# Performance work log

Measured on AMD Instinct MI355X. Metric: run time of the kernel, lower is better.

The kernel has to match this reference:

```python
import jax, jax.numpy as jnp
import numpy as np

INPUT_DIM = 512


def setup_inputs() -> dict:
    key = jax.random.key(0)
    ks = jax.random.split(key, 9)
    B = 262144
    d = INPUT_DIM
    inp = {
        "combined": jax.random.normal(ks[0], (B, 2 * d), dtype=jnp.float32),
        "W_in": jax.random.normal(ks[1], (d, 128), dtype=jnp.float32) / np.sqrt(d),
        "b_in": jax.random.normal(ks[2], (128,), dtype=jnp.float32) * 0.01,
        "W1": jax.random.normal(ks[3], (128, 128), dtype=jnp.float32) / np.sqrt(128.0),
        "b1": jax.random.normal(ks[4], (128,), dtype=jnp.float32) * 0.01,
        "W2": jax.random.normal(ks[5], (128, 64), dtype=jnp.float32) / np.sqrt(128.0),
        "b2": jax.random.normal(ks[6], (64,), dtype=jnp.float32) * 0.01,
        "W_out": jax.random.normal(ks[7], (128, 1), dtype=jnp.float32) / np.sqrt(128.0),
        "b_out": jax.random.normal(ks[8], (1,), dtype=jnp.float32) * 0.01,
    }
    return inp


def reference(combined, W_in, b_in, W1, b1, W2, b2, W_out, b_out):
    d = INPUT_DIM
    # Build per-sample 2-node graphs: nodes = (subj, obj). Shape [B, 2, d]
    x = jnp.stack([combined[:, :d], combined[:, d:]], axis=1)
    h = jax.nn.relu(x @ W_in + b_in)  # [B, 2, 128]

    # GCNConv on the 2-node graph (edges 0<->1 + default self-loops):
    # deg(i)=2, edge norm = 1/sqrt(2)*1/sqrt(2)=0.5, so both nodes get
    # 0.5*(h0 W + h1 W) + b == mean over nodes, transformed.
    def gcn(h, W, b):
        m = jnp.mean(h, axis=1, keepdims=True) @ W + b  # [B, 1, out]
        return jnp.broadcast_to(m, (h.shape[0], 2, W.shape[1]))

    h = jax.nn.relu(gcn(h, W1, b1))  # [B, 2, 128]
    h = jax.nn.relu(gcn(h, W2, b2))  # [B, 2, 64]

    combined_nodes = jnp.concatenate([h[:, 0], h[:, 1]], axis=-1)  # [B, 128]
    score = combined_nodes @ W_out + b_out  # [B, 1]
    return jax.nn.sigmoid(score)
```

## Files before the change

kernel.cpp:

```cpp
#include <hip/hip_runtime.h>
#include <hip/hip_bf16.h>
#include <cstdint>
#include <cstddef>


#define NROWS   524288
#define NSAMP   262144

typedef __attribute__((ext_vector_type(8))) short  bf16x8;
typedef __attribute__((ext_vector_type(4))) float  f32x4;

#define LGKM0() asm volatile("s_waitcnt lgkmcnt(0)" ::: "memory")

__device__ __forceinline__ unsigned short f2bf(float f) {
    unsigned u = __float_as_uint(f);
    u += 0x7fffu + ((u >> 16) & 1u);
    return (unsigned short)(u >> 16);
}

__device__ __forceinline__ bf16x8 cvt8(f32x4 lo, f32x4 hi) {
    union { unsigned u[4]; bf16x8 v; } r;
    asm("v_cvt_pk_bf16_f32 %0, %1, %2" : "=v"(r.u[0]) : "v"(lo[0]), "v"(lo[1]));
    asm("v_cvt_pk_bf16_f32 %0, %1, %2" : "=v"(r.u[1]) : "v"(lo[2]), "v"(lo[3]));
    asm("v_cvt_pk_bf16_f32 %0, %1, %2" : "=v"(r.u[2]) : "v"(hi[0]), "v"(hi[1]));
    asm("v_cvt_pk_bf16_f32 %0, %1, %2" : "=v"(r.u[3]) : "v"(hi[2]), "v"(hi[3]));
    return r.v;
}

__device__ __forceinline__ f32x4 mfma16(bf16x8 a, bf16x8 b, f32x4 c) {
    return __builtin_amdgcn_mfma_f32_16x16x32_bf16(a, b, c, 0, 0, 0);
}

#define WS_M     0
#define WS_WIN   67108864
#define WS_W1    67239936
#define WS_W2    67272704
#define WS_WEFF  67289088

__global__ void prep_kernel(const float* __restrict__ W_in,
                            const float* __restrict__ W1,
                            const float* __restrict__ W2,
                            const float* __restrict__ W_out,
                            unsigned short* __restrict__ fWin,
                            unsigned short* __restrict__ fW1,
                            unsigned short* __restrict__ fW2,
                            float* __restrict__ weff) {
    int tid = blockIdx.x * 256 + threadIdx.x;
    if (tid < 65536) {
        int e = tid;
        int j = e & 7, l = (e >> 3) & 63, rest = e >> 9;
        int n = rest & 7, kt = rest >> 3;
        int lg = l >> 4;
        int kin = (j < 4) ? (lg * 4 + j) : (16 + lg * 4 + (j - 4));
        int k = kt * 32 + kin;
        int col = n * 16 + (l & 15);
        fWin[e] = f2bf(W_in[k * 128 + col]);
    } else if (tid < 65536 + 16384) {
        int e = tid - 65536;
        int j = e & 7, l = (e >> 3) & 63, rest = e >> 9;
        int n = rest & 7, kt = rest >> 3;
        int k = kt * 32 + ((l >> 4) << 3) + j;
        int col = n * 16 + (l & 15);
        fW1[e] = f2bf(W1[k * 128 + col]);
    } else if (tid < 65536 + 16384 + 8192) {
        int e = tid - 65536 - 16384;
        int j = e & 7, l = (e >> 3) & 63, rest = e >> 9;
        int n = rest & 3, kt = rest >> 2;
        int k = kt * 32 + ((l >> 4) << 3) + j;
        int col = n * 16 + (l & 15);
        fW2[e] = f2bf(W2[k * 64 + col]);
    } else if (tid < 65536 + 16384 + 8192 + 64) {
        int c = tid - (65536 + 16384 + 8192);
        weff[c] = W_out[c] + W_out[64 + c];
    }
}

__global__ void __launch_bounds__(1024) __attribute__((amdgpu_waves_per_eu(4, 4)))
kA(const float* __restrict__ A,
   const unsigned short* __restrict__ fWin,
   const float* __restrict__ b_in,
   unsigned short* __restrict__ M) {
    __shared__ __align__(16) unsigned short lds[81920];
    unsigned short* lwin = lds;
    {
        const f32x4* src = (const f32x4*)fWin;
        f32x4* dst = (f32x4*)lds;
        int tid = threadIdx.x;
        #pragma unroll
        for (int i = 0; i < 8; ++i) dst[i * 1024 + tid] = src[i * 1024 + tid];
    }
    __syncthreads();
    const int w = threadIdx.x >> 6, l = threadIdx.x & 63;
    const int lr = l & 15, lg = l >> 4;
    char* bw = (char*)lds + 131072 + w * 2048;
    float binv[8];
    #pragma unroll
    for (int n = 0; n < 8; ++n) binv[n] = b_in[n * 16 + lr];

    const size_t NEXT = 131072;
    const float* a0 = A + ((size_t)blockIdx.x * 2048 + (size_t)w * 16 + lr) * 512 + lg * 4;

    f32x4 st[4][2];
    #pragma unroll
    for (int pc = 0; pc < 3; ++pc) {
        st[pc][0] = *(const f32x4*)(a0 + pc * 32);
        st[pc][1] = *(const f32x4*)(a0 + pc * 32 + 16);
    }

    for (int i = 0; i < 8; ++i) {
        const size_t nextoff = (i == 7) ? 0 : NEXT;
        f32x4 acc[8];
        #pragma unroll
        for (int n = 0; n < 8; ++n) acc[n] = (f32x4){0.f, 0.f, 0.f, 0.f};

        #pragma unroll
        for (int c = 0; c < 16; ++c) {
            {
                const int nb = (c + 3) & 3;
                const float* q0 = (c < 13) ? (a0 + (c + 3) * 32)
                                           : (a0 + nextoff + (c - 13) * 32);
                st[nb][0] = *(const f32x4*)(q0);
                st[nb][1] = *(const f32x4*)(q0 + 16);
            }
            const int cb = c & 3;
            bf16x8 af = cvt8(st[cb][0], st[cb][1]);
            #pragma unroll
            for (int n = 0; n < 8; ++n) {
                bf16x8 bf = *(const bf16x8*)&lwin[((c * 8 + n) * 64 + l) * 8];
                acc[n] = mfma16(af, bf, acc[n]);
            }
        }

        #pragma unroll
        for (int n = 0; n < 8; ++n) {
            const float b = binv[n];
            float h0 = fmaxf(acc[n][0] + b, 0.f);
            float h1 = fmaxf(acc[n][1] + b, 0.f);
            float h2 = fmaxf(acc[n][2] + b, 0.f);
            float h3 = fmaxf(acc[n][3] + b, 0.f);
            int bo = (2 * lg) * 256 + (n * 16 + lr) * 2;
            *(unsigned short*)(bw + bo)       = f2bf(0.5f * (h0 + h1));
            *(unsigned short*)(bw + bo + 256) = f2bf(0.5f * (h2 + h3));
        }
        LGKM0();
        const size_t sampbase = (size_t)blockIdx.x * 1024 + (size_t)i * 128 + (size_t)w * 8;
        #pragma unroll
        for (int r = 0; r < 2; ++r) {
            bf16x8 v = *(const bf16x8*)(bw + r * 1024 + l * 16);
            *(bf16x8*)&M[(sampbase + r * 4 + lg) * 128 + lr * 8] = v;
        }
        a0 += nextoff;
    }
}

__global__ void __launch_bounds__(256, 2)
kB(const unsigned short* __restrict__ M,
   const unsigned short* __restrict__ fW1,
   const unsigned short* __restrict__ fW2,
   const float* __restrict__ weff,
   const float* __restrict__ b1,
   const float* __restrict__ b2,
   const float* __restrict__ b_out,
   float* __restrict__ out) {
    __shared__ unsigned short lw1[16384];
    __shared__ unsigned short lw2[8192];
    __shared__ unsigned short bounce[4][2048];
    {
        int tid = threadIdx.x;
        const f32x4* s1 = (const f32x4*)fW1;
        f32x4* d1 = (f32x4*)lw1;
        #pragma unroll
        for (int i = 0; i < 8; ++i) d1[i * 256 + tid] = s1[i * 256 + tid];
        const f32x4* s2 = (const f32x4*)fW2;
        f32x4* d2 = (f32x4*)lw2;
        #pragma unroll
        for (int i = 0; i < 4; ++i) d2[i * 256 + tid] = s2[i * 256 + tid];
    }
    __syncthreads();
    const int w = threadIdx.x >> 6, l = threadIdx.x & 63;
    const int lr = l & 15, lg = l >> 4;
    float b1v[8], b2v[4], wev[4];
    #pragma unroll
    for (int n = 0; n < 8; ++n) b1v[n] = b1[n * 16 + lr];
    #pragma unroll
    for (int n = 0; n < 4; ++n) { b2v[n] = b2[n * 16 + lr]; wev[n] = weff[n * 16 + lr]; }
    const float bo = b_out[0];

    for (int t = blockIdx.x; t < NSAMP / 64; t += 512) {
        const int s0 = t * 64 + w * 16;
        f32x4 acc1[8];
        #pragma unroll
        for (int n = 0; n < 8; ++n) acc1[n] = (f32x4){0.f, 0.f, 0.f, 0.f};
        const unsigned short* arow = M + (size_t)(s0 + lr) * 128 + lg * 8;
        #pragma unroll
        for (int ks = 0; ks < 4; ++ks) {
            bf16x8 af = *(const bf16x8*)(arow + ks * 32);
            #pragma unroll
            for (int n = 0; n < 8; ++n) {
                bf16x8 bf = *(const bf16x8*)&lw1[((ks * 8 + n) * 64 + l) * 8];
                acc1[n] = __builtin_amdgcn_mfma_f32_16x16x32_bf16(af, bf, acc1[n], 0, 0, 0);
            }
        }
        #pragma unroll
        for (int n = 0; n < 8; ++n) {
            #pragma unroll
            for (int rr = 0; rr < 4; ++rr) {
                float g = fmaxf(acc1[n][rr] + b1v[n], 0.f);
                int row = lg * 4 + rr, col = n * 16 + lr;
                int boff = row * 256 + ((col * 2) ^ ((row & 7) << 4));
                bounce[w][boff >> 1] = f2bf(g);
            }
        }
        f32x4 acc2[4];
        #pragma unroll
        for (int n = 0; n < 4; ++n) acc2[n] = (f32x4){0.f, 0.f, 0.f, 0.f};
        #pragma unroll
        for (int ks = 0; ks < 4; ++ks) {
            int roff = lr * 256 + ((ks * 64 + lg * 16) ^ ((lr & 7) << 4));
            bf16x8 af2 = *(const bf16x8*)((const char*)&bounce[w][0] + roff);
            #pragma unroll
            for (int n = 0; n < 4; ++n) {
                bf16x8 bf = *(const bf16x8*)&lw2[((ks * 4 + n) * 64 + l) * 8];
                acc2[n] = __builtin_amdgcn_mfma_f32_16x16x32_bf16(af2, bf, acc2[n], 0, 0, 0);
            }
        }
        float p0 = 0.f, p1 = 0.f, p2 = 0.f, p3 = 0.f;
        #pragma unroll
        for (int n = 0; n < 4; ++n) {
            p0 += fmaxf(acc2[n][0] + b2v[n], 0.f) * wev[n];
            p1 += fmaxf(acc2[n][1] + b2v[n], 0.f) * wev[n];
            p2 += fmaxf(acc2[n][2] + b2v[n], 0.f) * wev[n];
            p3 += fmaxf(acc2[n][3] + b2v[n], 0.f) * wev[n];
        }
        #pragma unroll
        for (int m = 1; m < 16; m <<= 1) {
            p0 += __shfl_xor(p0, m);
            p1 += __shfl_xor(p1, m);
            p2 += __shfl_xor(p2, m);
            p3 += __shfl_xor(p3, m);
        }
        float s0f = 1.f / (1.f + expf(-(p0 + bo)));
        float s1f = 1.f / (1.f + expf(-(p1 + bo)));
        float s2f = 1.f / (1.f + expf(-(p2 + bo)));
        float s3f = 1.f / (1.f + expf(-(p3 + bo)));
        if (lr < 4) {
            float v = (lr == 0) ? s0f : (lr == 1) ? s1f : (lr == 2) ? s2f : s3f;
            out[s0 + lg * 4 + lr] = v;
        }
    }
}

extern "C" void kernel_launch(void* const* d_in, const int* in_sizes, int n_in,
                              void* d_out, int out_size, void* d_ws, size_t ws_size,
                              hipStream_t stream) {
    const float* combined = (const float*)d_in[0];
    const float* W_in  = (const float*)d_in[1];
    const float* b_in  = (const float*)d_in[2];
    const float* W1    = (const float*)d_in[3];
    const float* b1    = (const float*)d_in[4];
    const float* W2    = (const float*)d_in[5];
    const float* b2    = (const float*)d_in[6];
    const float* W_out = (const float*)d_in[7];
    const float* b_out = (const float*)d_in[8];
    float* out = (float*)d_out;

    char* ws = (char*)d_ws;
    unsigned short* M    = (unsigned short*)(ws + WS_M);
    unsigned short* fWin = (unsigned short*)(ws + WS_WIN);
    unsigned short* fW1  = (unsigned short*)(ws + WS_W1);
    unsigned short* fW2  = (unsigned short*)(ws + WS_W2);
    float* weff          = (float*)(ws + WS_WEFF);

    prep_kernel<<<(65536 + 16384 + 8192 + 64 + 255) / 256, 256, 0, stream>>>(
        W_in, W1, W2, W_out, fWin, fW1, fW2, weff);
    kA<<<256, 1024, 0, stream>>>(combined, fWin, b_in, M);
    kB<<<512, 256, 0, stream>>>(M, fW1, fW2, weff, b1, b2, b_out, out);
}
```

Before: 292.7 us.

## Stage input tiles through double-buffered swizzled LDS with register-resident W_in fragments

kA now uses 512-thread blocks. Each wave keeps its 16-column slice of W_in in registers, and the block cooperatively loads coalesced 32-row fp32 tiles, converts them to bf16 and stores them into double-buffered XOR-swizzled LDS. Each wave then reads its MFMA A fragments from LDS. The intermediate M is written in an MFMA-fragment order that kB reads with contiguous loads. The aim is to replace the strided per-lane global reads and repeated LDS weight reads with coalesced streaming, at the cost of a block barrier per tile and lower occupancy.

```diff
diff --git a/kernel.cpp b/kernel.cpp
--- a/kernel.cpp
+++ b/kernel.cpp
@@ -9,22 +9,16 @@
 
 typedef __attribute__((ext_vector_type(8))) short  bf16x8;
 typedef __attribute__((ext_vector_type(4))) float  f32x4;
+typedef __attribute__((ext_vector_type(2))) unsigned int u32x2;
 
 #define LGKM0() asm volatile("s_waitcnt lgkmcnt(0)" ::: "memory")
+#define VMW0()  asm volatile("s_waitcnt vmcnt(0)" ::: "memory")
+#define BAR()   __builtin_amdgcn_s_barrier()
 
 __device__ __forceinline__ unsigned short f2bf(float f) {
     unsigned u = __float_as_uint(f);
     u += 0x7fffu + ((u >> 16) & 1u);
     return (unsigned short)(u >> 16);
-}
-
-__device__ __forceinline__ bf16x8 cvt8(f32x4 lo, f32x4 hi) {
-    union { unsigned u[4]; bf16x8 v; } r;
-    asm("v_cvt_pk_bf16_f32 %0, %1, %2" : "=v"(r.u[0]) : "v"(lo[0]), "v"(lo[1]));
-    asm("v_cvt_pk_bf16_f32 %0, %1, %2" : "=v"(r.u[1]) : "v"(lo[2]), "v"(lo[3]));
-    asm("v_cvt_pk_bf16_f32 %0, %1, %2" : "=v"(r.u[2]) : "v"(hi[0]), "v"(hi[1]));
-    asm("v_cvt_pk_bf16_f32 %0, %1, %2" : "=v"(r.u[3]) : "v"(hi[2]), "v"(hi[3]));
-    return r.v;
 }
 
 __device__ __forceinline__ f32x4 mfma16(bf16x8 a, bf16x8 b, f32x4 c) {
@@ -50,9 +44,7 @@
         int e = tid;
         int j = e & 7, l = (e >> 3) & 63, rest = e >> 9;
         int n = rest & 7, kt = rest >> 3;
-        int lg = l >> 4;
-        int kin = (j < 4) ? (lg * 4 + j) : (16 + lg * 4 + (j - 4));
-        int k = kt * 32 + kin;
+        int k = kt * 32 + ((l >> 4) << 3) + j;
         int col = n * 16 + (l & 15);
         fWin[e] = f2bf(W_in[k * 128 + col]);
     } else if (tid < 65536 + 16384) {
@@ -75,86 +67,95 @@
     }
 }
 
-__global__ void __launch_bounds__(1024) __attribute__((amdgpu_waves_per_eu(4, 4)))
+__global__ void __launch_bounds__(512) __attribute__((amdgpu_waves_per_eu(2, 2)))
 kA(const float* __restrict__ A,
    const unsigned short* __restrict__ fWin,
    const float* __restrict__ b_in,
-   unsigned short* __restrict__ M) {
-    __shared__ __align__(16) unsigned short lds[81920];
-    unsigned short* lwin = lds;
-    {
-        const f32x4* src = (const f32x4*)fWin;
-        f32x4* dst = (f32x4*)lds;
-        int tid = threadIdx.x;
-        #pragma unroll
-        for (int i = 0; i < 8; ++i) dst[i * 1024 + tid] = src[i * 1024 + tid];
-    }
-    __syncthreads();
-    const int w = threadIdx.x >> 6, l = threadIdx.x & 63;
+   unsigned short* __restrict__ Mf) {
+    __shared__ __align__(16) char lds[73728];
+    char* buf0 = lds;
+    char* buf1 = lds + 32768;
+    char* bnc0 = lds + 65536;
+    char* bnc1 = lds + 69632;
+
+    const int tid = threadIdx.x, w = tid >> 6, l = tid & 63;
     const int lr = l & 15, lg = l >> 4;
-    char* bw = (char*)lds + 131072 + w * 2048;
-    float binv[8];
+
+    bf16x8 wfr[16];
     #pragma unroll
-    for (int n = 0; n < 8; ++n) binv[n] = b_in[n * 16 + lr];
-
-    const size_t NEXT = 131072;
-    const float* a0 = A + ((size_t)blockIdx.x * 2048 + (size_t)w * 16 + lr) * 512 + lg * 4;
-
-    f32x4 st[4][2];
-    #pragma unroll
-    for (int pc = 0; pc < 3; ++pc) {
-        st[pc][0] = *(const f32x4*)(a0 + pc * 32);
-        st[pc][1] = *(const f32x4*)(a0 + pc * 32 + 16);
-    }
-
-    for (int i = 0; i < 8; ++i) {
-        const size_t nextoff = (i == 7) ? 0 : NEXT;
-        f32x4 acc[8];
-        #pragma unroll
-        for (int n = 0; n < 8; ++n) acc[n] = (f32x4){0.f, 0.f, 0.f, 0.f};
-
-        #pragma unroll
-        for (int c = 0; c < 16; ++c) {
-            {
-                const int nb = (c + 3) & 3;
-                const float* q0 = (c < 13) ? (a0 + (c + 3) * 32)
-                                           : (a0 + nextoff + (c - 13) * 32);
-                st[nb][0] = *(const f32x4*)(q0);
-                st[nb][1] = *(const f32x4*)(q0 + 16);
-            }
-            const int cb = c & 3;
-            bf16x8 af = cvt8(st[cb][0], st[cb][1]);
-            #pragma unroll
-            for (int n = 0; n < 8; ++n) {
-                bf16x8 bf = *(const bf16x8*)&lwin[((c * 8 + n) * 64 + l) * 8];
-                acc[n] = mfma16(af, bf, acc[n]);
-            }
-        }
-
-        #pragma unroll
-        for (int n = 0; n < 8; ++n) {
-            const float b = binv[n];
-            float h0 = fmaxf(acc[n][0] + b, 0.f);
-            float h1 = fmaxf(acc[n][1] + b, 0.f);
-            float h2 = fmaxf(acc[n][2] + b, 0.f);
-            float h3 = fmaxf(acc[n][3] + b, 0.f);
-            int bo = (2 * lg) * 256 + (n * 16 + lr) * 2;
-            *(unsigned short*)(bw + bo)       = f2bf(0.5f * (h0 + h1));
-            *(unsigned short*)(bw + bo + 256) = f2bf(0.5f * (h2 + h3));
-        }
-        LGKM0();
-        const size_t sampbase = (size_t)blockIdx.x * 1024 + (size_t)i * 128 + (size_t)w * 8;
-        #pragma unroll
-        for (int r = 0; r < 2; ++r) {
-            bf16x8 v = *(const bf16x8*)(bw + r * 1024 + l * 16);
-            *(bf16x8*)&M[(sampbase + r * 4 + lg) * 128 + lr * 8] = v;
-        }
-        a0 += nextoff;
-    }
+    for (int kt = 0; kt < 16; ++kt)
+        wfr[kt] = *(const bf16x8*)&fWin[((kt * 8 + w) * 64 + l) * 8];
+    const float bb = b_in[w * 16 + lr];
+
+    const float* Ablk = A + (size_t)blockIdx.x * 2048 * 512;
+    const int lrow  = tid >> 7;
+    const int lcol2 = ((tid * 4) & 511) * 2;
+
+    f32x4 stg[8];
+    f32x4 acc0, acc1;
+
+    #define ISSUE(t) { const float* p = Ablk + (size_t)(t) * 16384 + tid * 4; \
+        _Pragma("unroll") for (int r = 0; r < 8; ++r) stg[r] = *(const f32x4*)(p + r * 2048); }
+    #define CVTWR(buf) { _Pragma("unroll") \
+        for (int r = 0; r < 8; ++r) { \
+            const int row = r * 4 + lrow; \
+            char* d = (buf) + row * 1024 + (lcol2 ^ ((row & 7) << 4)); \
+            unsigned pa, pb; \
+            asm("v_cvt_pk_bf16_f32 %0, %1, %2" : "=v"(pa) : "v"(stg[r][0]), "v"(stg[r][1])); \
+            asm("v_cvt_pk_bf16_f32 %0, %1, %2" : "=v"(pb) : "v"(stg[r][2]), "v"(stg[r][3])); \
+            u32x2 pk; pk[0] = pa; pk[1] = pb; \
+            *(u32x2*)d = pk; } }
+
+    ISSUE(0); VMW0(); CVTWR(buf0); LGKM0(); BAR();
+
+    for (int t = 0; t < 64; ++t) {
+        char* cur = (t & 1) ? buf1 : buf0;
+        char* nxt = (t & 1) ? buf0 : buf1;
+        char* bc  = (t & 1) ? bnc1 : bnc0;
+        if (t < 63) ISSUE(t + 1);
+
+        acc0 = (f32x4){0.f, 0.f, 0.f, 0.f};
+        acc1 = (f32x4){0.f, 0.f, 0.f, 0.f};
+        #pragma unroll
+        for (int kg = 0; kg < 16; ++kg) {
+            const int co = kg * 64 + lg * 16;
+            const int sw0 = co ^ ((lr & 7) << 4);
+            bf16x8 a0v = *(const bf16x8*)(cur + lr * 1024 + sw0);
+            bf16x8 a1v = *(const bf16x8*)(cur + (16 + lr) * 1024 + sw0);
+            acc0 = mfma16(a0v, wfr[kg], acc0);
+            acc1 = mfma16(a1v, wfr[kg], acc1);
+        }
+
+        {
+            const int c2 = (w * 16 + lr) * 2;
+            float m0 = 0.5f * (fmaxf(acc0[0] + bb, 0.f) + fmaxf(acc0[1] + bb, 0.f));
+            float m1 = 0.5f * (fmaxf(acc0[2] + bb, 0.f) + fmaxf(acc0[3] + bb, 0.f));
+            int s0 = 2 * lg, s1 = s0 + 1;
+            *(unsigned short*)(bc + s0 * 256 + (c2 ^ ((s0 & 7) << 4))) = f2bf(m0);
+            *(unsigned short*)(bc + s1 * 256 + (c2 ^ ((s1 & 7) << 4))) = f2bf(m1);
+            float m2 = 0.5f * (fmaxf(acc1[0] + bb, 0.f) + fmaxf(acc1[1] + bb, 0.f));
+            float m3 = 0.5f * (fmaxf(acc1[2] + bb, 0.f) + fmaxf(acc1[3] + bb, 0.f));
+            int s2 = 8 + 2 * lg, s3 = s2 + 1;
+            *(unsigned short*)(bc + s2 * 256 + (c2 ^ ((s2 & 7) << 4))) = f2bf(m2);
+            *(unsigned short*)(bc + s3 * 256 + (c2 ^ ((s3 & 7) << 4))) = f2bf(m3);
+        }
+
+        if (t < 63) { VMW0(); CVTWR(nxt); }
+        LGKM0(); BAR();
+
+        if (w < 4) {
+            int roff = lr * 256 + ((w * 64 + lg * 16) ^ ((lr & 7) << 4));
+            bf16x8 v = *(const bf16x8*)(bc + roff);
+            size_t F = (size_t)blockIdx.x * 64 + (size_t)t;
+            *(bf16x8*)&Mf[F * 2048 + (size_t)w * 512 + (size_t)l * 8] = v;
+        }
+    }
+    #undef ISSUE
+    #undef CVTWR
 }
 
 __global__ void __launch_bounds__(256, 2)
-kB(const unsigned short* __restrict__ M,
+kB(const unsigned short* __restrict__ Mf,
    const unsigned short* __restrict__ fW1,
    const unsigned short* __restrict__ fW2,
    const float* __restrict__ weff,
@@ -188,13 +189,13 @@
 
     for (int t = blockIdx.x; t < NSAMP / 64; t += 512) {
         const int s0 = t * 64 + w * 16;
+        const size_t F = (size_t)t * 4 + (size_t)w;
         f32x4 acc1[8];
         #pragma unroll
         for (int n = 0; n < 8; ++n) acc1[n] = (f32x4){0.f, 0.f, 0.f, 0.f};
-        const unsigned short* arow = M + (size_t)(s0 + lr) * 128 + lg * 8;
         #pragma unroll
         for (int ks = 0; ks < 4; ++ks) {
-            bf16x8 af = *(const bf16x8*)(arow + ks * 32);
+            bf16x8 af = *(const bf16x8*)&Mf[F * 2048 + ks * 512 + l * 8];
             #pragma unroll
             for (int n = 0; n < 8; ++n) {
                 bf16x8 bf = *(const bf16x8*)&lw1[((ks * 8 + n) * 64 + l) * 8];
@@ -265,7 +266,7 @@
     float* out = (float*)d_out;
 
     char* ws = (char*)d_ws;
-    unsigned short* M    = (unsigned short*)(ws + WS_M);
+    unsigned short* Mf   = (unsigned short*)(ws + WS_M);
     unsigned short* fWin = (unsigned short*)(ws + WS_WIN);
     unsigned short* fW1  = (unsigned short*)(ws + WS_W1);
     unsigned short* fW2  = (unsigned short*)(ws + WS_W2);
@@ -273,6 +274,6 @@
 
     prep_kernel<<<(65536 + 16384 + 8192 + 64 + 255) / 256, 256, 0, stream>>>(
         W_in, W1, W2, W_out, fWin, fW1, fW2, weff);
-    kA<<<256, 1024, 0, stream>>>(combined, fWin, b_in, M);
-    kB<<<512, 256, 0, stream>>>(M, fW1, fW2, weff, b1, b2, b_out, out);
-}
+    kA<<<256, 512, 0, stream>>>(combined, fWin, b_in, Mf);
+    kB<<<512, 256, 0, stream>>>(Mf, fW1, fW2, weff, b1, b2, b_out, out);
+}
```

New measurement: 307.6 us. 5.1% more time.
